# Kernel tuning notes

Measured on AMD Instinct MI355X. Metric: run time of the kernel, lower is better.

## Reference

```python
import jax, jax.numpy as jnp
import numpy as np

N, E = 50000, 800000
IN, MAP, H, O = 256, 64, 4, 64
LEAKY_SLOPE = 0.2


def setup_inputs() -> dict:
    key = jax.random.key(0)
    ks = jax.random.split(key, 12)
    x = jax.random.normal(ks[0], (N, IN), dtype=jnp.float32)
    src = jax.random.randint(ks[1], (E,), 0, N, dtype=jnp.int32)
    dst = jax.random.randint(ks[2], (E,), 0, N, dtype=jnp.int32)
    s = 1.0 / np.sqrt(IN)
    W_gat = jax.random.normal(ks[3], (IN, H * O), dtype=jnp.float32) * s
    attn_l = jax.random.normal(ks[4], (H, O), dtype=jnp.float32) * 0.1
    attn_r = jax.random.normal(ks[5], (H, O), dtype=jnp.float32) * 0.1
    gate_m_W = jax.random.normal(ks[6], (IN, MAP), dtype=jnp.float32) * s
    gate_m_b = jnp.zeros((MAP,), dtype=jnp.float32)
    gate_fn_W = jax.random.normal(ks[7], (2 * IN + MAP, H), dtype=jnp.float32) * (1.0 / np.sqrt(2 * IN + MAP))
    gate_fn_b = jnp.zeros((H,), dtype=jnp.float32)
    merge_W = jax.random.normal(ks[8], (IN + O, O), dtype=jnp.float32) * (1.0 / np.sqrt(IN + O))
    merge_b = jnp.zeros((O,), dtype=jnp.float32)
    return {"x": x, "src": src, "dst": dst, "W_gat": W_gat, "attn_l": attn_l,
            "attn_r": attn_r, "gate_m_W": gate_m_W, "gate_m_b": gate_m_b,
            "gate_fn_W": gate_fn_W, "gate_fn_b": gate_fn_b,
            "merge_W": merge_W, "merge_b": merge_b}


def _forward(x, src, dst, W_gat, attn_l, attn_r, gate_m_W, gate_m_b,
             gate_fn_W, gate_fn_b, merge_W, merge_b):
    n = x.shape[0]
    # --- gate branch: gspmm mean of x, gspmm max of linear_z over in-neighbors ---
    deg = jax.ops.segment_sum(jnp.ones_like(dst, dtype=x.dtype), dst, num_segments=n)
    mean_z = jax.ops.segment_sum(x[src], dst, num_segments=n) / jnp.maximum(deg, 1.0)[:, None]
    z = x @ gate_m_W + gate_m_b  # [N, MAP]
    max_z = jax.ops.segment_max(z[src], dst, num_segments=n)
    max_z = jnp.where(deg[:, None] > 0, max_z, 0.0)  # empty neighborhoods -> 0
    nft = jnp.concatenate([x, max_z, mean_z], axis=1)  # [N, 2*IN+MAP]
    gate = jax.nn.sigmoid(nft @ gate_fn_W + gate_fn_b)  # [N, H]
    # --- GATConv ---
    feat = (x @ W_gat).reshape(n, H, O)  # [N, H, O]
    el = jnp.einsum('nho,ho->nh', feat, attn_l)
    er = jnp.einsum('nho,ho->nh', feat, attn_r)
    e = jax.nn.leaky_relu(el[src] + er[dst], negative_slope=LEAKY_SLOPE)  # [E, H]
    m = jax.ops.segment_max(e, dst, num_segments=n)  # [N, H]
    m = jnp.where(jnp.isfinite(m), m, 0.0)
    ex = jnp.exp(e - m[dst])  # [E, H]
    s = jax.ops.segment_sum(ex, dst, num_segments=n)  # [N, H]
    alpha = ex / jnp.maximum(s[dst], 1e-16)  # [E, H]
    attn_out = jax.ops.segment_sum(feat[src] * alpha[:, :, None], dst, num_segments=n)  # [N, H, O]
    # --- gated merge ---
    gated = (gate[:, :, None] * attn_out).mean(axis=1)  # [N, O]
    merge = jnp.concatenate([x, gated], axis=1) @ merge_W + merge_b  # [N, O]
    return merge


def reference(x, src, dst, W_gat, attn_l, attn_r, gate_m_W, gate_m_b,
              gate_fn_W, gate_fn_b, merge_W, merge_b):
    return _forward(x, src, dst, W_gat, attn_l, attn_r, gate_m_W, gate_m_b,
                    gate_fn_W, gate_fn_b, merge_W, merge_b)
```

## Files before the change

### kernel.cpp

```cpp
#include <hip/hip_runtime.h>
#include <hip/hip_fp16.h>
#include <math.h>

#define NN 50000
#define NE 800000
#define LEAKY 0.2f
#define NT 26
#define CAP 96
#define NBT (8 * NT * 64)
#define NRB 3125
#define PACK_BLKS 6250
#define BT_BLKS 54
#define INIT_BLKS 196

typedef short bf16x8 __attribute__((ext_vector_type(8)));
typedef float f32x4 __attribute__((ext_vector_type(4)));
typedef float f32x2 __attribute__((ext_vector_type(2)));

__device__ __forceinline__ unsigned short f2bf(float f) {
  unsigned u = __float_as_uint(f);
  u += 0x7fffu + ((u >> 16) & 1u);
  return (unsigned short)(u >> 16);
}
__device__ __forceinline__ float leaky(float v) { return v > 0.0f ? v : LEAKY * v; }
__device__ __forceinline__ float rlf(float v, int l) {
  return __uint_as_float(__builtin_amdgcn_readlane(__float_as_uint(v), l));
}
__device__ __forceinline__ int rli(int v, int l) {
  return __builtin_amdgcn_readlane(v, l);
}
__device__ __forceinline__ int h2i(__half2 h) { union { __half2 h; int i; } u; u.h = h; return u.i; }
__device__ __forceinline__ __half2 i2h(int i) { union { __half2 h; int i; } u; u.i = i; return u.h; }

#if defined(__has_builtin)
#if __has_builtin(__builtin_amdgcn_cvt_pk_f32_fp8) && \
    __has_builtin(__builtin_amdgcn_cvt_pk_fp8_f32) && \
    __has_builtin(__builtin_amdgcn_cvt_f32_fp8)
#define FP8_HW 1
#endif
#endif

#ifdef FP8_HW
__device__ __forceinline__ unsigned char f2fp8(float v) {
  return (unsigned char)(__builtin_amdgcn_cvt_pk_fp8_f32(v, v, 0u, false) & 0xFF);
}
__device__ __forceinline__ f32x2 fp8x2_lo(unsigned int v) {
  return __builtin_amdgcn_cvt_pk_f32_fp8(v, false);
}
__device__ __forceinline__ f32x2 fp8x2_hi(unsigned int v) {
  return __builtin_amdgcn_cvt_pk_f32_fp8(v, true);
}
__device__ __forceinline__ float fp8one(unsigned int v) {
  return __builtin_amdgcn_cvt_f32_fp8(v, 0);
}
#else
__device__ __forceinline__ unsigned char f2fp8(float f) {
  unsigned u = __float_as_uint(f);
  unsigned s = (u >> 31) << 7;
  unsigned a = u & 0x7FFFFFFFu;
  if (a >= 0x43E00000u) return (unsigned char)(s | 0x7E);
  if (a < 0x3C800000u) {
    float m = __uint_as_float(a) * 512.0f;
    int q = (int)(m + 0.5f); if (q > 7) q = 7;
    return (unsigned char)(s | q);
  }
  a += 0x7FFFFu + ((a >> 20) & 1);
  unsigned e = ((a >> 23) & 0xFF) - 120;
  if (e > 15) return (unsigned char)(s | 0x7E);
  return (unsigned char)(s | (e << 3) | ((a >> 20) & 7));
}
__device__ __forceinline__ float fp8dec1(unsigned b) {
  unsigned s = (b & 0x80u) << 24;
  unsigned em = b & 0x7Fu;
  unsigned e4 = em >> 3, m3 = em & 7;
  float v = e4 ? __uint_as_float(((e4 + 120) << 23) | (m3 << 20))
               : (float)m3 * 0.001953125f;
  return __uint_as_float(__float_as_uint(v) ^ s);
}
__device__ __forceinline__ f32x2 fp8x2_lo(unsigned int v) {
  f32x2 r; r[0] = fp8dec1(v & 0xFF); r[1] = fp8dec1((v >> 8) & 0xFF); return r;
}
__device__ __forceinline__ f32x2 fp8x2_hi(unsigned int v) {
  f32x2 r; r[0] = fp8dec1((v >> 16) & 0xFF); r[1] = fp8dec1((v >> 24) & 0xFF); return r;
}
__device__ __forceinline__ float fp8one(unsigned int v) { return fp8dec1(v & 0xFF); }
#endif

__device__ __forceinline__ float panel_w(int col, int k,
    const float* W_gat, const float* gate_m_W, const float* merge_W,
    const float* gate_fn_W) {
  if (col < 256)      return W_gat[k * 256 + (col & 3) * 64 + (col >> 2)];
  else if (col < 320) return gate_m_W[k * 64 + (col - 256)];
  else if (col < 384) return merge_W[k * 64 + (col - 320)];
  else if (col < 388) return gate_fn_W[k * 4 + (col - 384)];
  else if (col < 392) return gate_fn_W[(320 + k) * 4 + (col - 388)];
  return 0.0f;
}

__global__ __launch_bounds__(256) void k_prep(
    const float* __restrict__ x, const float* __restrict__ W_gat,
    const float* __restrict__ gate_m_W, const float* __restrict__ merge_W,
    const float* __restrict__ gate_fn_W,
    unsigned short* __restrict__ xf, unsigned short* __restrict__ Btf,
    unsigned short* __restrict__ mWf,
    int* __restrict__ cursor, unsigned char* __restrict__ zq,
    float* __restrict__ epay) {
  int b = blockIdx.x, tid = threadIdx.x;
  if (b < PACK_BLKS) {
    int gid = b * 256 + tid;
    int rowblk = gid >> 9;
    int rem = gid & 511;
    int kq = rem >> 6, lane = rem & 63;
    int m = lane & 15, kg = lane >> 4;
    const float* p = x + (size_t)(rowblk * 16 + m) * 256 + kq * 32 + kg * 8;
    float4 fa = *(const float4*)p;
    float4 fb = *(const float4*)(p + 4);
    ushort4 o0, o1;
    o0.x = f2bf(fa.x); o0.y = f2bf(fa.y); o0.z = f2bf(fa.z); o0.w = f2bf(fa.w);
    o1.x = f2bf(fb.x); o1.y = f2bf(fb.y); o1.z = f2bf(fb.z); o1.w = f2bf(fb.w);
    ushort4* dst = (ushort4*)(xf + (size_t)gid * 8);
    dst[0] = o0; dst[1] = o1;
  } else if (b < PACK_BLKS + BT_BLKS) {
    int idx = (b - PACK_BLKS) * 256 + tid;
    if (idx < NBT) {
      int kq = idx / (NT * 64);
      int rem = idx - kq * (NT * 64);
      int t = rem >> 6, lane = rem & 63;
      int col = t * 16 + (lane & 15);
      int k = kq * 32 + (lane >> 4) * 8;
      unsigned short* o = Btf + (size_t)idx * 8;
#pragma unroll
      for (int i = 0; i < 8; ++i)
        o[i] = f2bf(panel_w(col, k + i, W_gat, gate_m_W, merge_W, gate_fn_W));
    } else if (idx < NBT + 512) {
      int idx2 = idx - NBT;
      int kq = idx2 >> 8;
      int rem = idx2 & 255;
      int t = rem >> 6, lane = rem & 63;
      int col = t * 16 + (lane & 15);
      int k = kq * 32 + ((lane >> 4) & 3) * 8;
      unsigned short* o = mWf + (size_t)idx2 * 8;
#pragma unroll
      for (int i = 0; i < 8; ++i)
        o[i] = f2bf(merge_W[(size_t)(256 + k + i) * 64 + col]);
    }
  } else {
    int i = (b - PACK_BLKS - BT_BLKS) * 256 + tid;
    if (i < NN) cursor[i] = 0;
    if (b == PACK_BLKS + BT_BLKS) {
      if (tid < 64) zq[(size_t)NN * 64 + tid] = 0xFE;
      if (tid < 8) epay[(size_t)NN * 8 + tid] = 0.0f;
    }
  }
}

__global__ void k_scatter(const int* __restrict__ src, const int* __restrict__ dst,
                          int* __restrict__ cursor, unsigned short* __restrict__ csr_src) {
  int e = blockIdx.x * 256 + threadIdx.x;
  if (e < NE) {
    int n = dst[e];
    int pos = atomicAdd(&cursor[n], 1);
    if (pos < CAP) csr_src[n * CAP + pos] = (unsigned short)src[e];
  }
}

__global__ __launch_bounds__(256) void k_gemm_mfma(
    const unsigned short* __restrict__ xf, const unsigned short* __restrict__ Btf,
    const float* __restrict__ gate_m_b,
    const float* __restrict__ attn_l, const float* __restrict__ attn_r,
    unsigned char* __restrict__ featq, unsigned char* __restrict__ zq,
    float* __restrict__ xm, float* __restrict__ gx, float* __restrict__ epay,
    float* __restrict__ erv) {
  __shared__ float els[32][4][2];
  __shared__ float ers[32][4][2];
  int lane = threadIdx.x & 63;
  int wave = threadIdx.x >> 6;
  int rowHalf = wave >> 1, colHalf = wave & 1;
  int rowB = blockIdx.x * 32;
  int row0 = rowB + rowHalf * 16;
  int t0 = colHalf * 13;
  int m = lane & 15;
  int kg = lane >> 4;
  f32x4 zero = {0.f, 0.f, 0.f, 0.f};
  f32x4 acc[13];
#pragma unroll
  for (int t = 0; t < 13; ++t) acc[t] = zero;

  const unsigned short* aB = xf + ((size_t)(blockIdx.x * 2 + rowHalf) * 8 * 64 + lane) * 8;
  const unsigned short* bB = Btf + (size_t)(t0 * 64 + lane) * 8;

  bf16x8 a0, a1, b0[13], b1[13];
  a0 = *(const bf16x8*)(aB);
#pragma unroll
  for (int t = 0; t < 13; ++t)
    b0[t] = *(const bf16x8*)(bB + (size_t)t * 64 * 8);
#pragma unroll 1
  for (int kq = 0; kq < 8; kq += 2) {
    a1 = *(const bf16x8*)(aB + (size_t)(kq + 1) * 64 * 8);
#pragma unroll
    for (int t = 0; t < 13; ++t)
      b1[t] = *(const bf16x8*)(bB + ((size_t)(kq + 1) * NT + t) * 64 * 8);
#pragma unroll
    for (int t = 0; t < 13; ++t)
      acc[t] = __builtin_amdgcn_mfma_f32_16x16x32_bf16(a0, b0[t], acc[t], 0, 0, 0);
    int kq2 = kq + 2 < 8 ? kq + 2 : 7;
    a0 = *(const bf16x8*)(aB + (size_t)kq2 * 64 * 8);
#pragma unroll
    for (int t = 0; t < 13; ++t)
      b0[t] = *(const bf16x8*)(bB + ((size_t)kq2 * NT + t) * 64 * 8);
#pragma unroll
    for (int t = 0; t < 13; ++t)
      acc[t] = __builtin_amdgcn_mfma_f32_16x16x32_bf16(a1, b1[t], acc[t], 0, 0, 0);
  }

  int h = m & 3, od = m >> 2;
  float elp[4] = {0, 0, 0, 0}, erp[4] = {0, 0, 0, 0};
#pragma unroll
  for (int t = 0; t < 13; ++t) {
    if ((t0 + t) * 16 < 256) {
      int o = (t0 + t) * 4 + od;
      float al = attn_l[h * 64 + o];
      float ar = attn_r[h * 64 + o];
#pragma unroll
      for (int r = 0; r < 4; ++r) {
        elp[r] += acc[t][r] * al;
        erp[r] += acc[t][r] * ar;
      }
    }
  }
#pragma unroll
  for (int r = 0; r < 4; ++r) {
    elp[r] += __shfl_xor(elp[r], 4, 64); elp[r] += __shfl_xor(elp[r], 8, 64);
    erp[r] += __shfl_xor(erp[r], 4, 64); erp[r] += __shfl_xor(erp[r], 8, 64);
  }
  if (m < 4) {
#pragma unroll
    for (int r = 0; r < 4; ++r) {
      els[rowHalf * 16 + kg * 4 + r][m][colHalf] = elp[r];
      ers[rowHalf * 16 + kg * 4 + r][m][colHalf] = erp[r];
    }
  }

  if (colHalf == 0) {
#pragma unroll
    for (int r = 0; r < 4; ++r) {
      int row = row0 + kg * 4 + r;
      if (row >= NN) continue;
#pragma unroll
      for (int t = 0; t < 13; ++t)
        featq[(size_t)row * 256 + t * 16 + m] = f2fp8(acc[t][r]);
    }
  } else {
#pragma unroll
    for (int r = 0; r < 4; ++r) {
      int row = row0 + kg * 4 + r;
      if (row >= NN) continue;
#pragma unroll
      for (int t = 0; t < 3; ++t)
        featq[(size_t)row * 256 + 208 + t * 16 + m] = f2fp8(acc[t][r]);
#pragma unroll
      for (int t = 3; t < 7; ++t) {
        int cc = (t - 3) * 16 + m;
        zq[(size_t)row * 64 + cc] = f2fp8(acc[t][r] + gate_m_b[cc]);
      }
#pragma unroll
      for (int t = 7; t < 11; ++t)
        xm[(size_t)row * 64 + (t - 7) * 16 + m] = acc[t][r];
      if (m < 4) gx[(size_t)row * 4 + m] = acc[11][r];
      else if (m < 8) epay[(size_t)row * 8 + (m - 4) * 2 + 1] = acc[11][r];
    }
  }
  __syncthreads();
  int tid = threadIdx.x;
  if (tid < 128) {
    int rr = tid >> 2, h2 = tid & 3;
    int row = rowB + rr;
    if (row < NN) {
      epay[(size_t)row * 8 + h2 * 2] = els[rr][h2][0] + els[rr][h2][1];
      erv[(size_t)row * 4 + h2] = ers[rr][h2][0] + ers[rr][h2][1];
    }
  }
}

__global__ __launch_bounds__(256) void k_node(
    const unsigned char* __restrict__ zq, const unsigned char* __restrict__ featq,
    const float* __restrict__ epay, const float* __restrict__ er,
    const float* __restrict__ gx,
    const int* __restrict__ cursor, const unsigned short* __restrict__ csr_src,
    const float* __restrict__ gate_fn_W, const float* __restrict__ gate_fn_b,
    unsigned short* __restrict__ gatedb) {
  __shared__ float WzT[4][64];
  int tid = threadIdx.x;
  {
    int c = tid >> 2, h = tid & 3;
    WzT[h][c] = gate_fn_W[(256 + c) * 4 + h];
  }
  __syncthreads();

  int lane = tid & 63;
  int node = blockIdx.x * 4 + (tid >> 6);
  if (node >= NN) return;
  int deg = cursor[node]; if (deg > CAP) deg = CAP;
  if (deg == 0) {
    gatedb[(size_t)node * 64 + lane] = 0;
    return;
  }
  int rs = node * CAP, re = rs + deg;
  int hh = lane >> 4, le = lane & 15;
  float er_h = er[(size_t)node * 4 + hh];

  __half2 a01 = __floats2half2_rn(0.f, 0.f);
  __half2 a23 = __floats2half2_rn(0.f, 0.f);
  float psum = 0, usum = 0;
  float mz = -INFINITY;
  for (int j0 = rs; j0 < re; j0 += 16) {
    int jj = j0 + le;
    bool valid = jj < re;
    int s_l = valid ? (int)csr_src[jj] : NN;
    float2 eu = *(const float2*)(epay + ((size_t)(unsigned)s_l << 3) + hh * 2);
    float lg = leaky(eu.x + er_h);
    float p = valid ? __expf(lg) : 0.0f;
    psum += p;
    usum += valid ? eu.y : 0.0f;
    float p0v = __shfl(p, le, 64);
    float p1v = __shfl(p, le + 16, 64);
    float p2v = __shfl(p, le + 32, 64);
    float p3v = __shfl(p, le + 48, 64);
    int pk01i = h2i(__floats2half2_rn(p0v, p1v));
    int pk23i = h2i(__floats2half2_rn(p2v, p3v));
#pragma unroll
    for (int e2 = 0; e2 < 16; ++e2) {
      int s = rli(s_l, e2);
      __half2 b01 = i2h(rli(pk01i, e2));
      __half2 b23 = i2h(rli(pk23i, e2));
      unsigned int fv = *(const unsigned int*)(featq + ((size_t)(unsigned)s << 8) + lane * 4);
      unsigned int zv = zq[((size_t)(unsigned)s << 6) + lane];
      f32x2 lo = fp8x2_lo(fv);
      f32x2 hi = fp8x2_hi(fv);
      __half2 h01 = __floats2half2_rn(lo[0], lo[1]);
      __half2 h23 = __floats2half2_rn(hi[0], hi[1]);
      a01 = __hfma2(b01, h01, a01);
      a23 = __hfma2(b23, h23, a23);
      mz = fmaxf(mz, fp8one(zv));
    }
  }
  float a0 = __low2float(a01), a1 = __high2float(a01);
  float a2 = __low2float(a23), a3 = __high2float(a23);
#pragma unroll
  for (int off = 1; off < 16; off <<= 1) {
    psum += __shfl_xor(psum, off, 64);
    usum += __shfl_xor(usum, off, 64);
  }
  float s0 = rlf(psum, 0),  s1 = rlf(psum, 16);
  float s2 = rlf(psum, 32), s3 = rlf(psum, 48);
  float su0 = rlf(usum, 0),  su1 = rlf(usum, 16);
  float su2 = rlf(usum, 32), su3 = rlf(usum, 48);

  float g[4];
#pragma unroll
  for (int h = 0; h < 4; ++h) {
    float t = mz * WzT[h][lane];
#pragma unroll
    for (int off = 32; off; off >>= 1) t += __shfl_xor(t, off, 64);
    g[h] = t;
  }
  float inv_deg = 1.0f / (float)deg;
  float4 gx4 = *(const float4*)(gx + (size_t)node * 4);
  float g0 = 1.0f / (1.0f + __expf(-(g[0] + gx4.x + su0 * inv_deg + gate_fn_b[0])));
  float g1 = 1.0f / (1.0f + __expf(-(g[1] + gx4.y + su1 * inv_deg + gate_fn_b[1])));
  float g2 = 1.0f / (1.0f + __expf(-(g[2] + gx4.z + su2 * inv_deg + gate_fn_b[2])));
  float g3 = 1.0f / (1.0f + __expf(-(g[3] + gx4.w + su3 * inv_deg + gate_fn_b[3])));

  float gated = 0.25f * (g0 * a0 / s0 + g1 * a1 / s1 + g2 * a2 / s2 + g3 * a3 / s3);
  gatedb[(size_t)node * 64 + lane] = f2bf(gated);
}

__global__ __launch_bounds__(256) void k_merge(
    const unsigned short* __restrict__ gatedb, const unsigned short* __restrict__ mWf,
    const float* __restrict__ xm, const float* __restrict__ merge_b,
    float* __restrict__ out) {
  int lane = threadIdx.x & 63;
  int wave = threadIdx.x >> 6;
  int row0 = blockIdx.x * 64 + wave * 16;
  int m = lane & 15;
  int kg = lane >> 4;
  f32x4 zero = {0.f, 0.f, 0.f, 0.f};
  f32x4 acc[4] = {zero, zero, zero, zero};
  int arow = row0 + m; if (arow >= NN) arow = NN - 1;
  const unsigned short* ap = gatedb + (size_t)arow * 64 + kg * 8;
#pragma unroll
  for (int kq = 0; kq < 2; ++kq) {
    bf16x8 a = *(const bf16x8*)(ap + kq * 32);
#pragma unroll
    for (int t = 0; t < 4; ++t) {
      bf16x8 b = *(const bf16x8*)(mWf + (((size_t)kq * 4 + t) * 64 + lane) * 8);
      acc[t] = __builtin_amdgcn_mfma_f32_16x16x32_bf16(a, b, acc[t], 0, 0, 0);
    }
  }
#pragma unroll
  for (int r = 0; r < 4; ++r) {
    int row = row0 + kg * 4 + r;
    if (row >= NN) continue;
#pragma unroll
    for (int t = 0; t < 4; ++t) {
      int c = t * 16 + m;
      out[(size_t)row * 64 + c] = acc[t][r] + xm[(size_t)row * 64 + c] + merge_b[c];
    }
  }
}

extern "C" void kernel_launch(void* const* d_in, const int* in_sizes, int n_in,
                              void* d_out, int out_size, void* d_ws, size_t ws_size,
                              hipStream_t stream) {
  const float* x         = (const float*)d_in[0];
  const int*   src       = (const int*)d_in[1];
  const int*   dst       = (const int*)d_in[2];
  const float* W_gat     = (const float*)d_in[3];
  const float* attn_l    = (const float*)d_in[4];
  const float* attn_r    = (const float*)d_in[5];
  const float* gate_m_W  = (const float*)d_in[6];
  const float* gate_m_b  = (const float*)d_in[7];
  const float* gate_fn_W = (const float*)d_in[8];
  const float* gate_fn_b = (const float*)d_in[9];
  const float* merge_W   = (const float*)d_in[10];
  const float* merge_b   = (const float*)d_in[11];
  float* out = (float*)d_out;

  char* ws = (char*)d_ws;
  size_t off = 0;
  auto alloc = [&](size_t bytes) -> void* {
    off = (off + 255) & ~(size_t)255;
    void* p = ws + off;
    off += bytes;
    return p;
  };
  int* cursor    = (int*)alloc((size_t)NN * 4);
  unsigned short* csr_src = (unsigned short*)alloc((size_t)NN * CAP * 2);
  float* epay = (float*)alloc((size_t)(NN + 1) * 8 * 4);
  float* er   = (float*)alloc((size_t)NN * 4 * 4);
  float* gx   = (float*)alloc((size_t)NN * 4 * 4);
  float* xm   = (float*)alloc((size_t)NN * 64 * 4);
  unsigned char* zq    = (unsigned char*)alloc((size_t)(NN + 1) * 64);
  unsigned char* featq = (unsigned char*)alloc((size_t)(NN + 1) * 256);
  unsigned short* gatedb = (unsigned short*)alloc((size_t)NN * 64 * 2);
  unsigned short* xf     = (unsigned short*)alloc((size_t)(NRB + 1) * 512 * 8 * 2);
  unsigned short* Btf    = (unsigned short*)alloc((size_t)NBT * 8 * 2);
  unsigned short* mWf    = (unsigned short*)alloc((size_t)512 * 8 * 2);

  k_prep<<<PACK_BLKS + BT_BLKS + INIT_BLKS, 256, 0, stream>>>(
      x, W_gat, gate_m_W, merge_W, gate_fn_W, xf, Btf, mWf, cursor, zq, epay);
  k_scatter<<<(NE + 255) / 256, 256, 0, stream>>>(src, dst, cursor, csr_src);
  k_gemm_mfma<<<(NN + 31) / 32, 256, 0, stream>>>(xf, Btf, gate_m_b, attn_l, attn_r,
                                                  featq, zq, xm, gx, epay, er);
  k_node<<<(NN + 3) / 4, 256, 0, stream>>>(zq, featq, epay, er, gx, cursor, csr_src,
                                           gate_fn_W, gate_fn_b, gatedb);
  k_merge<<<(NN + 63) / 64, 256, 0, stream>>>(gatedb, mWf, xm, merge_b, out);
}
```

Before: 265.8 us.

## Fuse merge GEMM into node kernel, double GEMM row tile, use fp32 aggregation

The node aggregation kernel now handles 16 nodes per block, four per wave. It stages the bf16 gated vectors in LDS and does the merge MFMA plus bias and residual in the same kernel. This removes the separate merge launch and the gatedb round trip through global memory. The projection GEMM now computes 64 rows per block with two accumulator groups that share each B fragment, with launch bounds of 2. It also grows the xf padding to cover the last block. Aggregation switches from half2 packed FMAs to fp32 FMAs with attention weights broadcast through LDS. This may add instruction and LDS traffic, and more GEMM registers may lower occupancy.

```diff
diff --git a/kernel.cpp b/kernel.cpp
--- a/kernel.cpp
+++ b/kernel.cpp
@@ -1,5 +1,4 @@
 #include <hip/hip_runtime.h>
-#include <hip/hip_fp16.h>
 #include <math.h>
 
 #define NN 50000
@@ -29,8 +28,6 @@
 __device__ __forceinline__ int rli(int v, int l) {
   return __builtin_amdgcn_readlane(v, l);
 }
-__device__ __forceinline__ int h2i(__half2 h) { union { __half2 h; int i; } u; u.h = h; return u.i; }
-__device__ __forceinline__ __half2 i2h(int i) { union { __half2 h; int i; } u; u.i = i; return u.h; }
 
 #if defined(__has_builtin)
 #if __has_builtin(__builtin_amdgcn_cvt_pk_f32_fp8) && \
@@ -164,57 +161,68 @@
   }
 }
 
-__global__ __launch_bounds__(256) void k_gemm_mfma(
+__global__ __launch_bounds__(256, 2) void k_gemm_mfma(
     const unsigned short* __restrict__ xf, const unsigned short* __restrict__ Btf,
     const float* __restrict__ gate_m_b,
     const float* __restrict__ attn_l, const float* __restrict__ attn_r,
     unsigned char* __restrict__ featq, unsigned char* __restrict__ zq,
     float* __restrict__ xm, float* __restrict__ gx, float* __restrict__ epay,
     float* __restrict__ erv) {
-  __shared__ float els[32][4][2];
-  __shared__ float ers[32][4][2];
+  __shared__ float els[64][4][2];
+  __shared__ float ers[64][4][2];
   int lane = threadIdx.x & 63;
   int wave = threadIdx.x >> 6;
   int rowHalf = wave >> 1, colHalf = wave & 1;
-  int rowB = blockIdx.x * 32;
-  int row0 = rowB + rowHalf * 16;
+  int rowB = blockIdx.x * 64;
+  int row0 = rowB + rowHalf * 32;
   int t0 = colHalf * 13;
-  int m = lane & 15;
-  int kg = lane >> 4;
+  int m = lane & 15, kg = lane >> 4;
   f32x4 zero = {0.f, 0.f, 0.f, 0.f};
-  f32x4 acc[13];
-#pragma unroll
-  for (int t = 0; t < 13; ++t) acc[t] = zero;
-
-  const unsigned short* aB = xf + ((size_t)(blockIdx.x * 2 + rowHalf) * 8 * 64 + lane) * 8;
+  f32x4 acc[2][13];
+#pragma unroll
+  for (int g = 0; g < 2; ++g)
+#pragma unroll
+    for (int t = 0; t < 13; ++t) acc[g][t] = zero;
+
+  const unsigned short* aB0 = xf + ((size_t)((blockIdx.x * 4 + rowHalf * 2) * 8) * 64 + lane) * 8;
+  const unsigned short* aB1 = aB0 + (size_t)8 * 64 * 8;
   const unsigned short* bB = Btf + (size_t)(t0 * 64 + lane) * 8;
 
-  bf16x8 a0, a1, b0[13], b1[13];
-  a0 = *(const bf16x8*)(aB);
+  bf16x8 aC0, aC1, aN0, aN1, bC[13], bN[13];
+  aC0 = *(const bf16x8*)(aB0);
+  aC1 = *(const bf16x8*)(aB1);
 #pragma unroll
   for (int t = 0; t < 13; ++t)
-    b0[t] = *(const bf16x8*)(bB + (size_t)t * 64 * 8);
+    bC[t] = *(const bf16x8*)(bB + (size_t)t * 512);
 #pragma unroll 1
   for (int kq = 0; kq < 8; kq += 2) {
-    a1 = *(const bf16x8*)(aB + (size_t)(kq + 1) * 64 * 8);
-#pragma unroll
-    for (int t = 0; t < 13; ++t)
-      b1[t] = *(const bf16x8*)(bB + ((size_t)(kq + 1) * NT + t) * 64 * 8);
-#pragma unroll
-    for (int t = 0; t < 13; ++t)
-      acc[t] = __builtin_amdgcn_mfma_f32_16x16x32_bf16(a0, b0[t], acc[t], 0, 0, 0);
+    aN0 = *(const bf16x8*)(aB0 + (size_t)(kq + 1) * 512);
+    aN1 = *(const bf16x8*)(aB1 + (size_t)(kq + 1) * 512);
+#pragma unroll
+    for (int t = 0; t < 13; ++t)
+      bN[t] = *(const bf16x8*)(bB + ((size_t)(kq + 1) * NT + t) * 512);
+#pragma unroll
+    for (int t = 0; t < 13; ++t)
+      acc[0][t] = __builtin_amdgcn_mfma_f32_16x16x32_bf16(aC0, bC[t], acc[0][t], 0, 0, 0);
+#pragma unroll
+    for (int t = 0; t < 13; ++t)
+      acc[1][t] = __builtin_amdgcn_mfma_f32_16x16x32_bf16(aC1, bC[t], acc[1][t], 0, 0, 0);
     int kq2 = kq + 2 < 8 ? kq + 2 : 7;
-    a0 = *(const bf16x8*)(aB + (size_t)kq2 * 64 * 8);
-#pragma unroll
-    for (int t = 0; t < 13; ++t)
-      b0[t] = *(const bf16x8*)(bB + ((size_t)kq2 * NT + t) * 64 * 8);
-#pragma unroll
-    for (int t = 0; t < 13; ++t)
-      acc[t] = __builtin_amdgcn_mfma_f32_16x16x32_bf16(a1, b1[t], acc[t], 0, 0, 0);
+    aC0 = *(const bf16x8*)(aB0 + (size_t)kq2 * 512);
+    aC1 = *(const bf16x8*)(aB1 + (size_t)kq2 * 512);
+#pragma unroll
+    for (int t = 0; t < 13; ++t)
+      bC[t] = *(const bf16x8*)(bB + ((size_t)kq2 * NT + t) * 512);
+#pragma unroll
+    for (int t = 0; t < 13; ++t)
+      acc[0][t] = __builtin_amdgcn_mfma_f32_16x16x32_bf16(aN0, bN[t], acc[0][t], 0, 0, 0);
+#pragma unroll
+    for (int t = 0; t < 13; ++t)
+      acc[1][t] = __builtin_amdgcn_mfma_f32_16x16x32_bf16(aN1, bN[t], acc[1][t], 0, 0, 0);
   }
 
   int h = m & 3, od = m >> 2;
-  float elp[4] = {0, 0, 0, 0}, erp[4] = {0, 0, 0, 0};
+  float elp[2][4] = {{0,0,0,0},{0,0,0,0}}, erp[2][4] = {{0,0,0,0},{0,0,0,0}};
 #pragma unroll
   for (int t = 0; t < 13; ++t) {
     if ((t0 + t) * 16 < 256) {
@@ -222,57 +230,66 @@
       float al = attn_l[h * 64 + o];
       float ar = attn_r[h * 64 + o];
 #pragma unroll
+      for (int g = 0; g < 2; ++g)
+#pragma unroll
+        for (int r = 0; r < 4; ++r) {
+          elp[g][r] += acc[g][t][r] * al;
+          erp[g][r] += acc[g][t][r] * ar;
+        }
+    }
+  }
+#pragma unroll
+  for (int g = 0; g < 2; ++g)
+#pragma unroll
+    for (int r = 0; r < 4; ++r) {
+      elp[g][r] += __shfl_xor(elp[g][r], 4, 64); elp[g][r] += __shfl_xor(elp[g][r], 8, 64);
+      erp[g][r] += __shfl_xor(erp[g][r], 4, 64); erp[g][r] += __shfl_xor(erp[g][r], 8, 64);
+    }
+  if (m < 4) {
+#pragma unroll
+    for (int g = 0; g < 2; ++g)
+#pragma unroll
       for (int r = 0; r < 4; ++r) {
-        elp[r] += acc[t][r] * al;
-        erp[r] += acc[t][r] * ar;
-      }
-    }
-  }
-#pragma unroll
-  for (int r = 0; r < 4; ++r) {
-    elp[r] += __shfl_xor(elp[r], 4, 64); elp[r] += __shfl_xor(elp[r], 8, 64);
-    erp[r] += __shfl_xor(erp[r], 4, 64); erp[r] += __shfl_xor(erp[r], 8, 64);
-  }
-  if (m < 4) {
-#pragma unroll
-    for (int r = 0; r < 4; ++r) {
-      els[rowHalf * 16 + kg * 4 + r][m][colHalf] = elp[r];
-      ers[rowHalf * 16 + kg * 4 + r][m][colHalf] = erp[r];
-    }
-  }
-
-  if (colHalf == 0) {
-#pragma unroll
-    for (int r = 0; r < 4; ++r) {
-      int row = row0 + kg * 4 + r;
-      if (row >= NN) continue;
-#pragma unroll
-      for (int t = 0; t < 13; ++t)
-        featq[(size_t)row * 256 + t * 16 + m] = f2fp8(acc[t][r]);
-    }
-  } else {
-#pragma unroll
-    for (int r = 0; r < 4; ++r) {
-      int row = row0 + kg * 4 + r;
-      if (row >= NN) continue;
-#pragma unroll
-      for (int t = 0; t < 3; ++t)
-        featq[(size_t)row * 256 + 208 + t * 16 + m] = f2fp8(acc[t][r]);
-#pragma unroll
-      for (int t = 3; t < 7; ++t) {
-        int cc = (t - 3) * 16 + m;
-        zq[(size_t)row * 64 + cc] = f2fp8(acc[t][r] + gate_m_b[cc]);
-      }
-#pragma unroll
-      for (int t = 7; t < 11; ++t)
-        xm[(size_t)row * 64 + (t - 7) * 16 + m] = acc[t][r];
-      if (m < 4) gx[(size_t)row * 4 + m] = acc[11][r];
-      else if (m < 8) epay[(size_t)row * 8 + (m - 4) * 2 + 1] = acc[11][r];
+        els[rowHalf * 32 + g * 16 + kg * 4 + r][m][colHalf] = elp[g][r];
+        ers[rowHalf * 32 + g * 16 + kg * 4 + r][m][colHalf] = erp[g][r];
+      }
+  }
+
+#pragma unroll
+  for (int g = 0; g < 2; ++g) {
+    if (colHalf == 0) {
+#pragma unroll
+      for (int r = 0; r < 4; ++r) {
+        int row = row0 + g * 16 + kg * 4 + r;
+        if (row >= NN) continue;
+#pragma unroll
+        for (int t = 0; t < 13; ++t)
+          featq[(size_t)row * 256 + t * 16 + m] = f2fp8(acc[g][t][r]);
+      }
+    } else {
+#pragma unroll
+      for (int r = 0; r < 4; ++r) {
+        int row = row0 + g * 16 + kg * 4 + r;
+        if (row >= NN) continue;
+#pragma unroll
+        for (int t = 0; t < 3; ++t)
+          featq[(size_t)row * 256 + 208 + t * 16 + m] = f2fp8(acc[g][t][r]);
+#pragma unroll
+        for (int t = 3; t < 7; ++t) {
+          int cc = (t - 3) * 16 + m;
+          zq[(size_t)row * 64 + cc] = f2fp8(acc[g][t][r] + gate_m_b[cc]);
+        }
+#pragma unroll
+        for (int t = 7; t < 11; ++t)
+          xm[(size_t)row * 64 + (t - 7) * 16 + m] = acc[g][t][r];
+        if (m < 4) gx[(size_t)row * 4 + m] = acc[g][11][r];
+        else if (m < 8) epay[(size_t)row * 8 + (m - 4) * 2 + 1] = acc[g][11][r];
+      }
     }
   }
   __syncthreads();
   int tid = threadIdx.x;
-  if (tid < 128) {
+  {
     int rr = tid >> 2, h2 = tid & 3;
     int row = rowB + rr;
     if (row < NN) {
@@ -288,8 +305,11 @@
     const float* __restrict__ gx,
     const int* __restrict__ cursor, const unsigned short* __restrict__ csr_src,
     const float* __restrict__ gate_fn_W, const float* __restrict__ gate_fn_b,
-    unsigned short* __restrict__ gatedb) {
+    const unsigned short* __restrict__ mWf, const float* __restrict__ xm,
+    const float* __restrict__ merge_b, float* __restrict__ out) {
   __shared__ float WzT[4][64];
+  __shared__ float pbuf[4][16][4];
+  __shared__ unsigned short gLDS[16][72];
   int tid = threadIdx.x;
   {
     int c = tid >> 2, h = tid & 3;
@@ -297,115 +317,88 @@
   }
   __syncthreads();
 
-  int lane = tid & 63;
-  int node = blockIdx.x * 4 + (tid >> 6);
-  if (node >= NN) return;
-  int deg = cursor[node]; if (deg > CAP) deg = CAP;
-  if (deg == 0) {
-    gatedb[(size_t)node * 64 + lane] = 0;
-    return;
-  }
-  int rs = node * CAP, re = rs + deg;
+  int lane = tid & 63, wave = tid >> 6;
   int hh = lane >> 4, le = lane & 15;
-  float er_h = er[(size_t)node * 4 + hh];
-
-  __half2 a01 = __floats2half2_rn(0.f, 0.f);
-  __half2 a23 = __floats2half2_rn(0.f, 0.f);
-  float psum = 0, usum = 0;
-  float mz = -INFINITY;
-  for (int j0 = rs; j0 < re; j0 += 16) {
-    int jj = j0 + le;
-    bool valid = jj < re;
-    int s_l = valid ? (int)csr_src[jj] : NN;
-    float2 eu = *(const float2*)(epay + ((size_t)(unsigned)s_l << 3) + hh * 2);
-    float lg = leaky(eu.x + er_h);
-    float p = valid ? __expf(lg) : 0.0f;
-    psum += p;
-    usum += valid ? eu.y : 0.0f;
-    float p0v = __shfl(p, le, 64);
-    float p1v = __shfl(p, le + 16, 64);
-    float p2v = __shfl(p, le + 32, 64);
-    float p3v = __shfl(p, le + 48, 64);
-    int pk01i = h2i(__floats2half2_rn(p0v, p1v));
-    int pk23i = h2i(__floats2half2_rn(p2v, p3v));
-#pragma unroll
-    for (int e2 = 0; e2 < 16; ++e2) {
-      int s = rli(s_l, e2);
-      __half2 b01 = i2h(rli(pk01i, e2));
-      __half2 b23 = i2h(rli(pk23i, e2));
-      unsigned int fv = *(const unsigned int*)(featq + ((size_t)(unsigned)s << 8) + lane * 4);
-      unsigned int zv = zq[((size_t)(unsigned)s << 6) + lane];
-      f32x2 lo = fp8x2_lo(fv);
-      f32x2 hi = fp8x2_hi(fv);
-      __half2 h01 = __floats2half2_rn(lo[0], lo[1]);
-      __half2 h23 = __floats2half2_rn(hi[0], hi[1]);
-      a01 = __hfma2(b01, h01, a01);
-      a23 = __hfma2(b23, h23, a23);
-      mz = fmaxf(mz, fp8one(zv));
-    }
-  }
-  float a0 = __low2float(a01), a1 = __high2float(a01);
-  float a2 = __low2float(a23), a3 = __high2float(a23);
-#pragma unroll
-  for (int off = 1; off < 16; off <<= 1) {
-    psum += __shfl_xor(psum, off, 64);
-    usum += __shfl_xor(usum, off, 64);
-  }
-  float s0 = rlf(psum, 0),  s1 = rlf(psum, 16);
-  float s2 = rlf(psum, 32), s3 = rlf(psum, 48);
-  float su0 = rlf(usum, 0),  su1 = rlf(usum, 16);
-  float su2 = rlf(usum, 32), su3 = rlf(usum, 48);
-
-  float g[4];
-#pragma unroll
-  for (int h = 0; h < 4; ++h) {
-    float t = mz * WzT[h][lane];
-#pragma unroll
-    for (int off = 32; off; off >>= 1) t += __shfl_xor(t, off, 64);
-    g[h] = t;
-  }
-  float inv_deg = 1.0f / (float)deg;
-  float4 gx4 = *(const float4*)(gx + (size_t)node * 4);
-  float g0 = 1.0f / (1.0f + __expf(-(g[0] + gx4.x + su0 * inv_deg + gate_fn_b[0])));
-  float g1 = 1.0f / (1.0f + __expf(-(g[1] + gx4.y + su1 * inv_deg + gate_fn_b[1])));
-  float g2 = 1.0f / (1.0f + __expf(-(g[2] + gx4.z + su2 * inv_deg + gate_fn_b[2])));
-  float g3 = 1.0f / (1.0f + __expf(-(g[3] + gx4.w + su3 * inv_deg + gate_fn_b[3])));
-
-  float gated = 0.25f * (g0 * a0 / s0 + g1 * a1 / s1 + g2 * a2 / s2 + g3 * a3 / s3);
-  gatedb[(size_t)node * 64 + lane] = f2bf(gated);
-}
-
-__global__ __launch_bounds__(256) void k_merge(
-    const unsigned short* __restrict__ gatedb, const unsigned short* __restrict__ mWf,
-    const float* __restrict__ xm, const float* __restrict__ merge_b,
-    float* __restrict__ out) {
-  int lane = threadIdx.x & 63;
-  int wave = threadIdx.x >> 6;
-  int row0 = blockIdx.x * 64 + wave * 16;
-  int m = lane & 15;
-  int kg = lane >> 4;
-  f32x4 zero = {0.f, 0.f, 0.f, 0.f};
-  f32x4 acc[4] = {zero, zero, zero, zero};
-  int arow = row0 + m; if (arow >= NN) arow = NN - 1;
-  const unsigned short* ap = gatedb + (size_t)arow * 64 + kg * 8;
+  int nodeBase = blockIdx.x * 16 + wave * 4;
+#pragma unroll 1
+  for (int i = 0; i < 4; ++i) {
+    int node = nodeBase + i;
+    int deg = cursor[node]; if (deg > CAP) deg = CAP;
+    float gated = 0.0f;
+    if (deg > 0) {
+      int rs = node * CAP, re = rs + deg;
+      float er_h = er[(size_t)node * 4 + hh];
+      float a0 = 0, a1 = 0, a2 = 0, a3 = 0;
+      float psum = 0, usum = 0;
+      float mz = -INFINITY;
+      for (int j0 = rs; j0 < re; j0 += 16) {
+        int jj = j0 + le;
+        bool valid = jj < re;
+        int s_l = valid ? (int)csr_src[jj] : NN;
+        float2 eu = *(const float2*)(epay + ((size_t)(unsigned)s_l << 3) + hh * 2);
+        float p = valid ? __expf(leaky(eu.x + er_h)) : 0.0f;
+        psum += p;
+        usum += valid ? eu.y : 0.0f;
+        pbuf[wave][le][hh] = p;
+#pragma unroll
+        for (int e2 = 0; e2 < 16; ++e2) {
+          int s = rli(s_l, e2);
+          float4 pv = *(const float4*)pbuf[wave][e2];
+          unsigned int fv = *(const unsigned int*)(featq + ((size_t)(unsigned)s << 8) + lane * 4);
+          unsigned int zv = zq[((size_t)(unsigned)s << 6) + lane];
+          f32x2 lo = fp8x2_lo(fv);
+          f32x2 hi = fp8x2_hi(fv);
+          a0 += pv.x * lo[0];
+          a1 += pv.y * lo[1];
+          a2 += pv.z * hi[0];
+          a3 += pv.w * hi[1];
+          mz = fmaxf(mz, fp8one(zv));
+        }
+      }
+#pragma unroll
+      for (int off = 1; off < 16; off <<= 1) {
+        psum += __shfl_xor(psum, off, 64);
+        usum += __shfl_xor(usum, off, 64);
+      }
+      float s0 = rlf(psum, 0),  s1 = rlf(psum, 16);
+      float s2 = rlf(psum, 32), s3 = rlf(psum, 48);
+      float su0 = rlf(usum, 0),  su1 = rlf(usum, 16);
+      float su2 = rlf(usum, 32), su3 = rlf(usum, 48);
+
+      float g[4];
+#pragma unroll
+      for (int h = 0; h < 4; ++h) {
+        float t = mz * WzT[h][lane];
+#pragma unroll
+        for (int off = 32; off; off >>= 1) t += __shfl_xor(t, off, 64);
+        g[h] = t;
+      }
+      float inv_deg = 1.0f / (float)deg;
+      float4 gx4 = *(const float4*)(gx + (size_t)node * 4);
+      float g0 = 1.0f / (1.0f + __expf(-(g[0] + gx4.x + su0 * inv_deg + gate_fn_b[0])));
+      float g1 = 1.0f / (1.0f + __expf(-(g[1] + gx4.y + su1 * inv_deg + gate_fn_b[1])));
+      float g2 = 1.0f / (1.0f + __expf(-(g[2] + gx4.z + su2 * inv_deg + gate_fn_b[2])));
+      float g3 = 1.0f / (1.0f + __expf(-(g[3] + gx4.w + su3 * inv_deg + gate_fn_b[3])));
+      gated = 0.25f * (g0 * a0 / s0 + g1 * a1 / s1 + g2 * a2 / s2 + g3 * a3 / s3);
+    }
+    gLDS[wave * 4 + i][lane] = f2bf(gated);
+  }
+  __syncthreads();
+
+  int m = lane & 15, kg = lane >> 4;
+  f32x4 acc = {0.f, 0.f, 0.f, 0.f};
 #pragma unroll
   for (int kq = 0; kq < 2; ++kq) {
-    bf16x8 a = *(const bf16x8*)(ap + kq * 32);
-#pragma unroll
-    for (int t = 0; t < 4; ++t) {
-      bf16x8 b = *(const bf16x8*)(mWf + (((size_t)kq * 4 + t) * 64 + lane) * 8);
-      acc[t] = __builtin_amdgcn_mfma_f32_16x16x32_bf16(a, b, acc[t], 0, 0, 0);
-    }
-  }
+    bf16x8 a = *(const bf16x8*)(&gLDS[m][kq * 32 + kg * 8]);
+    bf16x8 b = *(const bf16x8*)(mWf + (((size_t)kq * 4 + wave) * 64 + lane) * 8);
+    acc = __builtin_amdgcn_mfma_f32_16x16x32_bf16(a, b, acc, 0, 0, 0);
+  }
+  int c = wave * 16 + m;
+  float mb = merge_b[c];
 #pragma unroll
   for (int r = 0; r < 4; ++r) {
-    int row = row0 + kg * 4 + r;
-    if (row >= NN) continue;
-#pragma unroll
-    for (int t = 0; t < 4; ++t) {
-      int c = t * 16 + m;
-      out[(size_t)row * 64 + c] = acc[t][r] + xm[(size_t)row * 64 + c] + merge_b[c];
-    }
+    int row = blockIdx.x * 16 + kg * 4 + r;
+    out[(size_t)row * 64 + c] = acc[r] + xm[(size_t)row * 64 + c] + mb;
   }
 }
 
@@ -442,17 +435,15 @@
   float* xm   = (float*)alloc((size_t)NN * 64 * 4);
   unsigned char* zq    = (unsigned char*)alloc((size_t)(NN + 1) * 64);
   unsigned char* featq = (unsigned char*)alloc((size_t)(NN + 1) * 256);
-  unsigned short* gatedb = (unsigned short*)alloc((size_t)NN * 64 * 2);
-  unsigned short* xf     = (unsigned short*)alloc((size_t)(NRB + 1) * 512 * 8 * 2);
+  unsigned short* xf     = (unsigned short*)alloc((size_t)(NRB + 4) * 512 * 8 * 2);
   unsigned short* Btf    = (unsigned short*)alloc((size_t)NBT * 8 * 2);
   unsigned short* mWf    = (unsigned short*)alloc((size_t)512 * 8 * 2);
 
   k_prep<<<PACK_BLKS + BT_BLKS + INIT_BLKS, 256, 0, stream>>>(
       x, W_gat, gate_m_W, merge_W, gate_fn_W, xf, Btf, mWf, cursor, zq, epay);
   k_scatter<<<(NE + 255) / 256, 256, 0, stream>>>(src, dst, cursor, csr_src);
-  k_gemm_mfma<<<(NN + 31) / 32, 256, 0, stream>>>(xf, Btf, gate_m_b, attn_l, attn_r,
+  k_gemm_mfma<<<(NN + 63) / 64, 256, 0, stream>>>(xf, Btf, gate_m_b, attn_l, attn_r,
                                                   featq, zq, xm, gx, epay, er);
-  k_node<<<(NN + 3) / 4, 256, 0, stream>>>(zq, featq, epay, er, gx, cursor, csr_src,
-                                           gate_fn_W, gate_fn_b, gatedb);
-  k_merge<<<(NN + 63) / 64, 256, 0, stream>>>(gatedb, mWf, xm, merge_b, out);
-}
+  k_node<<<NN / 16, 256, 0, stream>>>(zq, featq, epay, er, gx, cursor, csr_src,
+                                      gate_fn_W, gate_fn_b, mWf, xm, merge_b, out);
+}
```

New measurement: 245.7 us. 7.5% less time.
